# Kernel tuning notes

Hardware: AMD Instinct MI355X
Metric: run time of the kernel (lower is better)

Reference implementation:

```python
import jax, jax.numpy as jnp
import numpy as np

N = 256        # ImageSize
NC = 8         # coils
NSPOKE = 34    # radial spokes
NVEC = 512     # samples per spoke
K = NSPOKE * NVEC  # total k-space points


def setup_inputs() -> dict:
    key = jax.random.key(0)
    k1, k2, k3, k4 = jax.random.split(key, 4)
    input_r = jax.random.normal(k1, (N, N, 2), dtype=jnp.float32)
    C_r = jax.random.normal(k2, (NC, N, N, 2), dtype=jnp.float32)
    w = jax.random.uniform(k3, (NVEC,), dtype=jnp.float32)
    # nonuniform k-space coordinates in [-pi, pi)
    angle = jax.random.uniform(k4, (K, 2), dtype=jnp.float32,
                               minval=-np.pi, maxval=np.pi)
    return {"input_r": input_r, "C_r": C_r, "w": w, "angle": angle}


def reference(input_r, C_r, w, angle):
    # Type-3 NUFFT: y[c,k] = sum_j C[c,j]*x[j] * exp(-i*(s_k*(-x1_j) + t_k*(-x2_j)))
    #             = sum_{a,b} (C[c,a,b]*x[a,b]) * exp(+i*s_k*g[a]) * exp(+i*t_k*g[b])
    # since the source grid is separable: x1_j = g[a], x2_j = g[b],
    # g = linspace(-N//2, N//2-1, N) for even N (iflag=0 -> negative sign).
    n = input_r.shape[0]
    nvec = w.shape[0]
    g = jnp.arange(n, dtype=jnp.float32) - n // 2          # [N]

    x = input_r[..., 0] + 1j * input_r[..., 1]             # [N,N] complex64
    C = C_r[..., 0] + 1j * C_r[..., 1]                     # [Nc,N,N] complex64
    Xc = C * x[None]                                       # coil-weighted image [Nc,N,N]

    s = angle[:, 0]                                        # [K]
    t = angle[:, 1]                                        # [K]
    E1 = jnp.exp(1j * s[:, None] * g[None, :])             # [K,N] phase along axis a
    E2 = jnp.exp(1j * t[:, None] * g[None, :])             # [K,N] phase along axis b

    # contract b first -> [Nc,K,N], then a -> [Nc,K]
    y = jnp.einsum('kb,cab,ka->ck', E2, Xc, E1, optimize=True)  # [Nc,K]

    # density compensation: wr = tile(w, (Nc, Nspoke, 1)).reshape(Nc, -1)
    wr = jnp.tile(w, y.shape[1] // nvec)                   # [K]
    y = y * wr[None, :]

    return jnp.stack([jnp.real(y), jnp.imag(y)], axis=-1)  # [Nc,K,2] float32
```

## Files before the change

kernel.cpp:

```cpp
#include <hip/hip_runtime.h>
#include <hip/hip_bf16.h>
#include <stdint.h>


#define NKTOT 17408
#define NBLK 272
#define NT 9

typedef short bf16x8 __attribute__((ext_vector_type(8)));
typedef float f32x4 __attribute__((ext_vector_type(4)));

__device__ __forceinline__ unsigned short f2bf(float f) {
  unsigned int u = __builtin_bit_cast(unsigned int, f);
  u += 0x7FFFu + ((u >> 16) & 1u);
  return (unsigned short)(u >> 16);
}
__device__ __forceinline__ float bf2f(unsigned int lo16) {
  return __builtin_bit_cast(float, lo16 << 16);
}

__device__ __forceinline__ void async_copy16(void* lds, const void* g) {
  __builtin_amdgcn_global_load_lds(
      (const __attribute__((address_space(1))) unsigned int*)g,
      (__attribute__((address_space(3))) unsigned int*)lds, 16, 0, 0);
}

__device__ __forceinline__ size_t aidx(int c, int m, int j) {
  int tt = j >> 5, p = m >> 1;
  int s = ((m & 1) << 2) | ((j >> 3) & 3);
  return ((size_t)((c * 9 + tt) * 256 + p)) * 64 + s * 8 + (j & 7);
}
__device__ __forceinline__ size_t bidx(int kt, int kl, int j) {
  int tt = j >> 5, p = kl >> 1;
  int s = ((kl & 1) << 2) | ((j >> 3) & 3);
  return ((size_t)((kt * 9 + tt) * 32 + p)) * 64 + s * 8 + (j & 7);
}

__global__ __launch_bounds__(256) void pack_all(
    const float* __restrict__ input_r, const float* __restrict__ C_r,
    const float* __restrict__ angle,
    unsigned short* __restrict__ Apack, unsigned short* __restrict__ BT,
    unsigned int* __restrict__ E1tab)
{
  const int bx = blockIdx.x;
  const int tid = threadIdx.x;
  if (bx < 1024) {
    const int p = bx * 2 + (tid >> 7);
    const int a = p & 255;
    const int c = p >> 8;
    const int j = tid & 127;
    const size_t xbase = (size_t)a * 256;
    const size_t cbase = ((size_t)(c * 256 + a)) * 256;
    const int mr = a, mi = 256 + a;
    if (j == 0) {
      float xr = input_r[(xbase + 128) * 2], xi = input_r[(xbase + 128) * 2 + 1];
      float cr = C_r[(cbase + 128) * 2],     ci = C_r[(cbase + 128) * 2 + 1];
      Apack[aidx(c, mr, 0)] = f2bf(cr * xr - ci * xi);
      Apack[aidx(c, mi, 0)] = f2bf(cr * xi + ci * xr);
      xr = input_r[xbase * 2]; xi = input_r[xbase * 2 + 1];
      cr = C_r[cbase * 2];     ci = C_r[cbase * 2 + 1];
      float reb = cr * xr - ci * xi, imb = cr * xi + ci * xr;
      Apack[aidx(c, mr, 128)] = f2bf(reb);
      Apack[aidx(c, mi, 128)] = f2bf(imb);
      Apack[aidx(c, mr, 256)] = f2bf(imb);
      Apack[aidx(c, mi, 256)] = f2bf(-reb);
    } else {
      const int bp = 128 + j, bm = 128 - j;
      float xpr = input_r[(xbase + bp) * 2], xpi = input_r[(xbase + bp) * 2 + 1];
      float cpr = C_r[(cbase + bp) * 2],     cpi = C_r[(cbase + bp) * 2 + 1];
      float pr = cpr * xpr - cpi * xpi, pi = cpr * xpi + cpi * xpr;
      float xmr = input_r[(xbase + bm) * 2], xmi = input_r[(xbase + bm) * 2 + 1];
      float cmr = C_r[(cbase + bm) * 2],     cmi = C_r[(cbase + bm) * 2 + 1];
      float mrv = cmr * xmr - cmi * xmi, miv = cmr * xmi + cmi * xmr;
      Apack[aidx(c, mr, j)]       = f2bf(pr + mrv);
      Apack[aidx(c, mi, j)]       = f2bf(pi + miv);
      Apack[aidx(c, mr, 128 + j)] = f2bf(miv - pi);
      Apack[aidx(c, mi, 128 + j)] = f2bf(pr - mrv);
    }
    if (j < 31) {
      Apack[aidx(c, mr, 257 + j)] = 0;
      Apack[aidx(c, mi, 257 + j)] = 0;
    }
  } else {
    const int k = bx - 1024;
    const int kt = k >> 6, kl = k & 63;
    const float s = angle[k * 2 + 0];
    const float t = angle[k * 2 + 1];
    float sn, cs;
    __sincosf(s * (float)(tid - 128), &sn, &cs);
    E1tab[(size_t)k * 256 + tid] =
        (unsigned int)f2bf(cs) | ((unsigned int)f2bf(sn) << 16);
    if (tid <= 128) {
      __sincosf(t * (float)tid, &sn, &cs);
      BT[bidx(kt, kl, tid)] = f2bf(cs);
      if (tid >= 1) BT[bidx(kt, kl, 128 + tid)] = f2bf(sn);
    } else if (tid < 160) {
      BT[bidx(kt, kl, 128 + tid)] = 0;
    }
  }
}

__global__ __launch_bounds__(256, 2) void gemm_fused(
    const unsigned short* __restrict__ Apack,
    const unsigned short* __restrict__ BT,
    const unsigned int* __restrict__ E1tab,
    const float* __restrict__ wvec,
    float* __restrict__ out)
{
  __shared__ unsigned short As[2][16384];
  __shared__ unsigned short Bs[2][2048];
  __shared__ float scol[4][2][64];

  const int bx = blockIdx.x;
  const int c = (bx >> 3) & 7;
  const int ktile = (bx >> 6) * 8 + (bx & 7);
  const int kt0 = ktile * 64;
  const int tid = threadIdx.x;
  const int w = tid >> 6;
  const int l = tid & 63;
  const int lhi = l >> 4;
  const int llo = l & 15;
  const int lr = l >> 3;
  const int lsw = ((l & 7) ^ lr) * 8;

  const unsigned short* Aimg = Apack + (size_t)c * 9 * 16384;
  const unsigned short* Bimg = BT + (size_t)ktile * 9 * 2048;

  const int u8 = (((((llo & 1) << 2) | lhi)) ^ (llo >> 1)) * 8;
  const int aprow = w * 64 + (llo >> 1);
  const int bprow = llo >> 1;

  f32x4 acc[8][4];
#pragma unroll
  for (int i = 0; i < 8; ++i)
#pragma unroll
    for (int j = 0; j < 4; ++j) {
      f32x4 z = {0.f, 0.f, 0.f, 0.f};
      acc[i][j] = z;
    }

#pragma unroll
  for (int i = 0; i < 8; ++i) {
    int row0 = (w * 8 + i) * 8;
    async_copy16(&As[0][row0 * 64], Aimg + (size_t)(row0 + lr) * 64 + lsw);
  }
  async_copy16(&Bs[0][w * 8 * 64], Bimg + (size_t)(w * 8 + lr) * 64 + lsw);
  __syncthreads();

#pragma unroll 2
  for (int tt = 0; tt < NT; ++tt) {
    const int cu = tt & 1;
    const unsigned short* Ac = As[cu];
    const unsigned short* Bc = Bs[cu];
    if (tt < NT - 1) {
      const unsigned short* Asrc = Aimg + (size_t)(tt + 1) * 16384;
      const unsigned short* Bsrc = Bimg + (size_t)(tt + 1) * 2048;
      unsigned short* An = As[cu ^ 1];
      unsigned short* Bn = Bs[cu ^ 1];
#pragma unroll
      for (int i = 0; i < 8; ++i) {
        int row0 = (w * 8 + i) * 8;
        async_copy16(&An[row0 * 64], Asrc + (size_t)(row0 + lr) * 64 + lsw);
      }
      async_copy16(&Bn[w * 8 * 64], Bsrc + (size_t)(w * 8 + lr) * 64 + lsw);
    }
    __builtin_amdgcn_sched_barrier(0);

    bf16x8 bfr[4];
#pragma unroll
    for (int fj = 0; fj < 4; ++fj)
      bfr[fj] = *(const bf16x8*)&Bc[(fj * 8 + bprow) * 64 + u8];
    bf16x8 af[8];
#pragma unroll
    for (int fi = 0; fi < 8; ++fi)
      af[fi] = *(const bf16x8*)&Ac[(aprow + fi * 8) * 64 + u8];
#pragma unroll
    for (int fi = 0; fi < 8; ++fi)
#pragma unroll
      for (int fj = 0; fj < 4; ++fj)
        acc[fi][fj] = __builtin_amdgcn_mfma_f32_16x16x32_bf16(
            af[fi], bfr[fj], acc[fi][fj], 0, 0, 0);
    __syncthreads();
  }

  const int ahalf = (w & 1) * 128;
#pragma unroll
  for (int fj = 0; fj < 4; ++fj) {
    const int col = fj * 16 + llo;
    const int k = kt0 + col;
    float sumr = 0.f, sumi = 0.f;
    const unsigned int* e1base = E1tab + (size_t)k * 256 + ahalf + lhi * 4;
#pragma unroll
    for (int fi = 0; fi < 8; ++fi) {
      uint4 e4 = *(const uint4*)(e1base + fi * 16);
      unsigned int ev[4] = {e4.x, e4.y, e4.z, e4.w};
#pragma unroll
      for (int r = 0; r < 4; ++r) {
        float v = acc[fi][fj][r];
        sumr += bf2f(ev[r] & 0xFFFFu) * v;
        sumi += bf2f(ev[r] >> 16) * v;
      }
    }
    sumr += __shfl_xor(sumr, 16, 64);
    sumr += __shfl_xor(sumr, 32, 64);
    sumi += __shfl_xor(sumi, 16, 64);
    sumi += __shfl_xor(sumi, 32, 64);
    if (lhi == 0) {
      scol[w][0][col] = sumr;
      scol[w][1][col] = sumi;
    }
  }
  __syncthreads();
  if (tid < 128) {
    const int col = tid >> 1;
    const int comp = tid & 1;
    const int k = kt0 + col;
    float re = scol[0][0][col] + scol[1][0][col]
             - scol[2][1][col] - scol[3][1][col];
    float im = scol[0][1][col] + scol[1][1][col]
             + scol[2][0][col] + scol[3][0][col];
    float val = comp ? im : re;
    out[((size_t)c * NKTOT + k) * 2 + comp] = val * wvec[k & 511];
  }
}

extern "C" void kernel_launch(void* const* d_in, const int* in_sizes, int n_in,
                              void* d_out, int out_size, void* d_ws, size_t ws_size,
                              hipStream_t stream) {
  const float* input_r = (const float*)d_in[0];
  const float* C_r     = (const float*)d_in[1];
  const float* wvec    = (const float*)d_in[2];
  const float* angle   = (const float*)d_in[3];
  float* out = (float*)d_out;

  unsigned short* Apack = (unsigned short*)d_ws;
  unsigned short* BT    = (unsigned short*)((char*)d_ws + (size_t)2359296);
  unsigned int*   E1tab = (unsigned int*)((char*)d_ws + (size_t)2359296 + 10027008);

  pack_all<<<1024 + NKTOT, 256, 0, stream>>>(input_r, C_r, angle,
                                             Apack, BT, E1tab);
  gemm_fused<<<8 * NBLK, 256, 0, stream>>>(Apack, BT, E1tab, wvec, out);
}
```

Before: 139.7 us.

## Trim GEMM K to 256 with fp32 bias init and per-wave A pipelines

The j=0 column of the contraction moves out of the bf16 GEMM into an fp32 bias table that initialises the accumulators. This cuts K from 288 to 256 (9 to 8 tiles) and drops the zero padding. Each wave now streams its own A slab into private LDS double buffers and waits with vmcnt instead of block-wide __syncthreads. B fragments are loaded straight from global memory into registers, double-buffered, rather than staged through LDS. This removes barrier stalls and a tile of MFMA work, at the cost of uncoalesced-ish global B reads and hand-tuned waitcnt correctness.

```diff
diff --git a/kernel.cpp b/kernel.cpp
--- a/kernel.cpp
+++ b/kernel.cpp
@@ -5,10 +5,13 @@
 
 #define NKTOT 17408
 #define NBLK 272
-#define NT 9
+#define NT 8
+#define LDB 256
 
 typedef short bf16x8 __attribute__((ext_vector_type(8)));
 typedef float f32x4 __attribute__((ext_vector_type(4)));
+
+#define WAITVM(N) asm volatile("s_waitcnt vmcnt(" #N ")" ::: "memory")
 
 __device__ __forceinline__ unsigned short f2bf(float f) {
   unsigned int u = __builtin_bit_cast(unsigned int, f);
@@ -25,22 +28,18 @@
       (__attribute__((address_space(3))) unsigned int*)lds, 16, 0, 0);
 }
 
-__device__ __forceinline__ size_t aidx(int c, int m, int j) {
-  int tt = j >> 5, p = m >> 1;
-  int s = ((m & 1) << 2) | ((j >> 3) & 3);
-  return ((size_t)((c * 9 + tt) * 256 + p)) * 64 + s * 8 + (j & 7);
-}
-__device__ __forceinline__ size_t bidx(int kt, int kl, int j) {
-  int tt = j >> 5, p = kl >> 1;
-  int s = ((kl & 1) << 2) | ((j >> 3) & 3);
-  return ((size_t)((kt * 9 + tt) * 32 + p)) * 64 + s * 8 + (j & 7);
+__device__ __forceinline__ size_t aidx(int c, int m, int jj) {
+  int w = m >> 7, ml = m & 127;
+  int tt = jj >> 5;
+  int s = ((ml & 1) << 2) | ((jj >> 3) & 3);
+  return ((((size_t)(c * 8 + tt) * 4 + w) * 64 + (ml >> 1)) * 8 + s) * 8 + (jj & 7);
 }
 
 __global__ __launch_bounds__(256) void pack_all(
     const float* __restrict__ input_r, const float* __restrict__ C_r,
     const float* __restrict__ angle,
     unsigned short* __restrict__ Apack, unsigned short* __restrict__ BT,
-    unsigned int* __restrict__ E1tab)
+    float* __restrict__ biastab, unsigned int* __restrict__ E1tab)
 {
   const int bx = blockIdx.x;
   const int tid = threadIdx.x;
@@ -51,19 +50,18 @@
     const int j = tid & 127;
     const size_t xbase = (size_t)a * 256;
     const size_t cbase = ((size_t)(c * 256 + a)) * 256;
-    const int mr = a, mi = 256 + a;
     if (j == 0) {
       float xr = input_r[(xbase + 128) * 2], xi = input_r[(xbase + 128) * 2 + 1];
       float cr = C_r[(cbase + 128) * 2],     ci = C_r[(cbase + 128) * 2 + 1];
-      Apack[aidx(c, mr, 0)] = f2bf(cr * xr - ci * xi);
-      Apack[aidx(c, mi, 0)] = f2bf(cr * xi + ci * xr);
+      biastab[c * 512 + a]       = cr * xr - ci * xi;
+      biastab[c * 512 + 256 + a] = cr * xi + ci * xr;
       xr = input_r[xbase * 2]; xi = input_r[xbase * 2 + 1];
       cr = C_r[cbase * 2];     ci = C_r[cbase * 2 + 1];
       float reb = cr * xr - ci * xi, imb = cr * xi + ci * xr;
-      Apack[aidx(c, mr, 128)] = f2bf(reb);
-      Apack[aidx(c, mi, 128)] = f2bf(imb);
-      Apack[aidx(c, mr, 256)] = f2bf(imb);
-      Apack[aidx(c, mi, 256)] = f2bf(-reb);
+      Apack[aidx(c, a, 127)]       = f2bf(reb);
+      Apack[aidx(c, a, 255)]       = f2bf(imb);
+      Apack[aidx(c, 256 + a, 127)] = f2bf(imb);
+      Apack[aidx(c, 256 + a, 255)] = f2bf(-reb);
     } else {
       const int bp = 128 + j, bm = 128 - j;
       float xpr = input_r[(xbase + bp) * 2], xpi = input_r[(xbase + bp) * 2 + 1];
@@ -72,30 +70,23 @@
       float xmr = input_r[(xbase + bm) * 2], xmi = input_r[(xbase + bm) * 2 + 1];
       float cmr = C_r[(cbase + bm) * 2],     cmi = C_r[(cbase + bm) * 2 + 1];
       float mrv = cmr * xmr - cmi * xmi, miv = cmr * xmi + cmi * xmr;
-      Apack[aidx(c, mr, j)]       = f2bf(pr + mrv);
-      Apack[aidx(c, mi, j)]       = f2bf(pi + miv);
-      Apack[aidx(c, mr, 128 + j)] = f2bf(miv - pi);
-      Apack[aidx(c, mi, 128 + j)] = f2bf(pr - mrv);
-    }
-    if (j < 31) {
-      Apack[aidx(c, mr, 257 + j)] = 0;
-      Apack[aidx(c, mi, 257 + j)] = 0;
+      Apack[aidx(c, a, j - 1)]           = f2bf(pr + mrv);
+      Apack[aidx(c, a, 127 + j)]         = f2bf(miv - pi);
+      Apack[aidx(c, 256 + a, j - 1)]     = f2bf(pi + miv);
+      Apack[aidx(c, 256 + a, 127 + j)]   = f2bf(pr - mrv);
     }
   } else {
     const int k = bx - 1024;
-    const int kt = k >> 6, kl = k & 63;
     const float s = angle[k * 2 + 0];
     const float t = angle[k * 2 + 1];
     float sn, cs;
     __sincosf(s * (float)(tid - 128), &sn, &cs);
     E1tab[(size_t)k * 256 + tid] =
         (unsigned int)f2bf(cs) | ((unsigned int)f2bf(sn) << 16);
-    if (tid <= 128) {
+    if (tid >= 1 && tid <= 128) {
       __sincosf(t * (float)tid, &sn, &cs);
-      BT[bidx(kt, kl, tid)] = f2bf(cs);
-      if (tid >= 1) BT[bidx(kt, kl, 128 + tid)] = f2bf(sn);
-    } else if (tid < 160) {
-      BT[bidx(kt, kl, 128 + tid)] = 0;
+      BT[(size_t)k * LDB + tid - 1]   = f2bf(cs);
+      BT[(size_t)k * LDB + 127 + tid] = f2bf(sn);
     }
   }
 }
@@ -103,12 +94,12 @@
 __global__ __launch_bounds__(256, 2) void gemm_fused(
     const unsigned short* __restrict__ Apack,
     const unsigned short* __restrict__ BT,
+    const float* __restrict__ biastab,
     const unsigned int* __restrict__ E1tab,
     const float* __restrict__ wvec,
     float* __restrict__ out)
 {
-  __shared__ unsigned short As[2][16384];
-  __shared__ unsigned short Bs[2][2048];
+  __shared__ unsigned short As[4][2][4096];
   __shared__ float scol[4][2][64];
 
   const int bx = blockIdx.x;
@@ -123,64 +114,59 @@
   const int lr = l >> 3;
   const int lsw = ((l & 7) ^ lr) * 8;
 
-  const unsigned short* Aimg = Apack + (size_t)c * 9 * 16384;
-  const unsigned short* Bimg = BT + (size_t)ktile * 9 * 2048;
-
-  const int u8 = (((((llo & 1) << 2) | lhi)) ^ (llo >> 1)) * 8;
-  const int aprow = w * 64 + (llo >> 1);
-  const int bprow = llo >> 1;
+  const unsigned short* Aimg = Apack + ((size_t)c * 32 + w) * 4096;
+  const unsigned short* Bw = BT + ((size_t)kt0 + llo) * LDB + lhi * 8;
+  const float* biasp = biastab + c * 512 + w * 128 + lhi * 4;
+
+  const int u8 = (((((llo & 1) << 2) | lhi)) ^ ((llo >> 1) & 7)) * 8;
+  const int plbase = (llo >> 1);
 
   f32x4 acc[8][4];
+  bf16x8 bfrag[2][4];
+
 #pragma unroll
   for (int i = 0; i < 8; ++i)
-#pragma unroll
-    for (int j = 0; j < 4; ++j) {
-      f32x4 z = {0.f, 0.f, 0.f, 0.f};
-      acc[i][j] = z;
-    }
-
-#pragma unroll
-  for (int i = 0; i < 8; ++i) {
-    int row0 = (w * 8 + i) * 8;
-    async_copy16(&As[0][row0 * 64], Aimg + (size_t)(row0 + lr) * 64 + lsw);
-  }
-  async_copy16(&Bs[0][w * 8 * 64], Bimg + (size_t)(w * 8 + lr) * 64 + lsw);
-  __syncthreads();
-
-#pragma unroll 2
-  for (int tt = 0; tt < NT; ++tt) {
-    const int cu = tt & 1;
-    const unsigned short* Ac = As[cu];
-    const unsigned short* Bc = Bs[cu];
-    if (tt < NT - 1) {
-      const unsigned short* Asrc = Aimg + (size_t)(tt + 1) * 16384;
-      const unsigned short* Bsrc = Bimg + (size_t)(tt + 1) * 2048;
-      unsigned short* An = As[cu ^ 1];
-      unsigned short* Bn = Bs[cu ^ 1];
-#pragma unroll
-      for (int i = 0; i < 8; ++i) {
-        int row0 = (w * 8 + i) * 8;
-        async_copy16(&An[row0 * 64], Asrc + (size_t)(row0 + lr) * 64 + lsw);
-      }
-      async_copy16(&Bn[w * 8 * 64], Bsrc + (size_t)(w * 8 + lr) * 64 + lsw);
-    }
+    async_copy16(&As[w][0][i * 512], Aimg + (size_t)(i * 8 + lr) * 64 + lsw);
+#pragma unroll
+  for (int fj = 0; fj < 4; ++fj)
+    bfrag[0][fj] = *(const bf16x8*)(Bw + (size_t)fj * 16 * LDB);
+#pragma unroll
+  for (int fi = 0; fi < 8; ++fi) {
+    f32x4 b4 = *(const f32x4*)(biasp + fi * 16);
+#pragma unroll
+    for (int fj = 0; fj < 4; ++fj) acc[fi][fj] = b4;
+  }
+
+#pragma unroll
+  for (int t = 0; t < NT; ++t) {
+    const int cu = t & 1;
+    const int nx = cu ^ 1;
     __builtin_amdgcn_sched_barrier(0);
-
-    bf16x8 bfr[4];
-#pragma unroll
-    for (int fj = 0; fj < 4; ++fj)
-      bfr[fj] = *(const bf16x8*)&Bc[(fj * 8 + bprow) * 64 + u8];
+    if (t < NT - 1) {
+#pragma unroll
+      for (int i = 0; i < 8; ++i)
+        async_copy16(&As[w][nx][i * 512],
+                     Aimg + (size_t)(t + 1) * 16384 + (i * 8 + lr) * 64 + lsw);
+#pragma unroll
+      for (int fj = 0; fj < 4; ++fj)
+        bfrag[nx][fj] = *(const bf16x8*)(Bw + (size_t)fj * 16 * LDB + (t + 1) * 32);
+      __builtin_amdgcn_sched_barrier(0);
+      WAITVM(12);
+    } else {
+      __builtin_amdgcn_sched_barrier(0);
+      WAITVM(0);
+    }
+    __builtin_amdgcn_sched_barrier(0);
     bf16x8 af[8];
 #pragma unroll
     for (int fi = 0; fi < 8; ++fi)
-      af[fi] = *(const bf16x8*)&Ac[(aprow + fi * 8) * 64 + u8];
+      af[fi] = *(const bf16x8*)&As[w][cu][(fi * 8 + plbase) * 64 + u8];
 #pragma unroll
     for (int fi = 0; fi < 8; ++fi)
 #pragma unroll
       for (int fj = 0; fj < 4; ++fj)
         acc[fi][fj] = __builtin_amdgcn_mfma_f32_16x16x32_bf16(
-            af[fi], bfr[fj], acc[fi][fj], 0, 0, 0);
-    __syncthreads();
+            af[fi], bfrag[cu][fj], acc[fi][fj], 0, 0, 0);
   }
 
   const int ahalf = (w & 1) * 128;
@@ -234,10 +220,11 @@
   float* out = (float*)d_out;
 
   unsigned short* Apack = (unsigned short*)d_ws;
-  unsigned short* BT    = (unsigned short*)((char*)d_ws + (size_t)2359296);
-  unsigned int*   E1tab = (unsigned int*)((char*)d_ws + (size_t)2359296 + 10027008);
+  unsigned short* BT    = (unsigned short*)((char*)d_ws + (size_t)2097152);
+  float*          biastab = (float*)((char*)d_ws + (size_t)2097152 + 8912896);
+  unsigned int*   E1tab = (unsigned int*)((char*)d_ws + (size_t)2097152 + 8912896 + 16384);
 
   pack_all<<<1024 + NKTOT, 256, 0, stream>>>(input_r, C_r, angle,
-                                             Apack, BT, E1tab);
-  gemm_fused<<<8 * NBLK, 256, 0, stream>>>(Apack, BT, E1tab, wvec, out);
-}
+                                             Apack, BT, biastab, E1tab);
+  gemm_fused<<<8 * NBLK, 256, 0, stream>>>(Apack, BT, biastab, E1tab, wvec, out);
+}
```

Result: slower. 154.0 us (+10.2%).
